# Optimization experiments

Hardware: AMD Instinct MI355X
Metric: run time of the kernel (lower is better)

Reference implementation:

```python
import jax, jax.numpy as jnp
import numpy as np

BETA = 0.25
EPS = 1e-12


def l2_normalize(x, axis=-1, eps=EPS):
    return x * jax.lax.rsqrt((x * x).sum(axis=axis, keepdims=True) + eps)


def setup_inputs() -> dict:
    key = jax.random.key(0)
    k1, k2 = jax.random.split(key)
    z = jax.random.normal(k1, (16, 32, 32, 256), dtype=jnp.float32)
    # embedding_init = uniform(2.0, -1.0) -> U[-1, 1)
    embedding = jax.random.uniform(k2, (8192, 256), dtype=jnp.float32) * 2.0 - 1.0
    return {"z": z, "embedding": embedding}


def reference(z, embedding):
    e_dim = embedding.shape[-1]
    z_flat = jnp.reshape(z, (-1, e_dim))                      # [N, D]
    z_flat_n = l2_normalize(z_flat, axis=-1)                  # [N, D]
    emb_n = l2_normalize(embedding, axis=-1)                  # [K, D]
    # squared L2 distance between normalized vectors
    d = (jnp.sum(z_flat_n ** 2, axis=1, keepdims=True)
         + jnp.sum(emb_n ** 2, axis=1)
         - 2.0 * jnp.einsum('nd,kd->nk', z_flat_n, emb_n))    # [N, K]
    min_idx = jnp.reshape(jnp.argmin(d, axis=1), z.shape[:-1])  # [B,H,W]
    # codebook lookup + renormalize
    z_q = l2_normalize(jnp.take(embedding, min_idx, axis=0), axis=-1)  # [B,H,W,D]
    z_norm = l2_normalize(z, axis=-1)
    loss = (BETA * jnp.mean(jnp.square(jax.lax.stop_gradient(z_q) - z_norm))
            + jnp.mean(jnp.square(z_q - jax.lax.stop_gradient(z_norm))))
    # straight-through estimator
    z_q_st = z + jax.lax.stop_gradient(z_q - z)
    return (z_q_st, loss, min_idx)
```

## Files before the change

kernel.cpp:

```cpp
#include <hip/hip_runtime.h>
#include <math.h>

#define D 256
#define NROW 16384
#define KCODE 8192
#define MARGIN 1.2e-3f

typedef _Float16 half8 __attribute__((ext_vector_type(8)));
typedef _Float16 half4f __attribute__((ext_vector_type(4)));
typedef __attribute__((ext_vector_type(4))) float f32x4;

__device__ __forceinline__ float dot4(float4 a, float4 b) {
  return a.x * b.x + a.y * b.y + a.z * b.z + a.w * b.w;
}
__device__ __forceinline__ float wave_sum(float s) {
#pragma unroll
  for (int off = 32; off; off >>= 1) s += __shfl_xor(s, off, 64);
  return s;
}
__device__ __forceinline__ float wave_min_f(float v) {
#pragma unroll
  for (int off = 32; off; off >>= 1) v = fminf(v, __shfl_xor(v, off, 64));
  return v;
}

__global__ __launch_bounds__(256) void k_prep(const float* __restrict__ emb,
                                              const float* __restrict__ z,
                                              float* __restrict__ emb_n,
                                              float* __restrict__ e2,
                                              _Float16* __restrict__ Bb,
                                              _Float16* __restrict__ Ab) {
  const int b = blockIdx.x;
  const int w = threadIdx.x >> 6, l = threadIdx.x & 63;
  const int ph = l >> 3;
  const int qd = (l & 7) >> 1;
  const int hf = l & 1;
  if (b < 2048) {
    int row = b * 4 + w;
    float4 v = ((const float4*)(emb + (size_t)row * D))[l];
    float s = wave_sum(dot4(v, v));
    float inv = 1.0f / sqrtf(s + 1e-12f);
    v.x *= inv; v.y *= inv; v.z *= inv; v.w *= inv;
    ((float4*)(emb_n + (size_t)row * D))[l] = v;
    float s2 = wave_sum(dot4(v, v));
    if (l == 0) e2[row] = s2;
    half4f h;
    h[0] = (_Float16)v.x; h[1] = (_Float16)v.y;
    h[2] = (_Float16)v.z; h[3] = (_Float16)v.w;
    int t = row >> 7, r = row & 127;
    size_t off = (size_t)t * 32768 + ph * 4096 + (r >> 6) * 2048 +
                 ((r >> 4) & 3) * 512 + (qd * 16 + (r & 15)) * 8 + hf * 4;
    *(half4f*)(Bb + off) = h;
  } else {
    int row = (b - 2048) * 4 + w;
    float4 v = ((const float4*)(z + (size_t)row * D))[l];
    float s = wave_sum(dot4(v, v));
    float inv = 1.0f / sqrtf(s + 1e-12f);
    v.x *= inv; v.y *= inv; v.z *= inv; v.w *= inv;
    half4f h;
    h[0] = (_Float16)v.x; h[1] = (_Float16)v.y;
    h[2] = (_Float16)v.z; h[3] = (_Float16)v.w;
    int t = row >> 7, r = row & 127;
    size_t off = (size_t)t * 32768 + ph * 4096 + (r >> 6) * 2048 +
                 ((r >> 4) & 3) * 512 + (qd * 16 + (r & 15)) * 8 + hf * 4;
    *(half4f*)(Ab + off) = h;
  }
}

__device__ __forceinline__ void merge2(float& d1, int& k1, float& d2, int& k2,
                                       float od1, int ok1, float od2, int ok2) {
  bool w1 = (od1 < d1) || (od1 == d1 && ok1 < k1);
  float n1 = w1 ? od1 : d1; int nk1 = w1 ? ok1 : k1;
  float c  = w1 ? d1 : od1; int ck  = w1 ? k1 : ok1;
  float c2 = w1 ? od2 : d2; int ck2 = w1 ? ok2 : k2;
  bool w2 = (c2 < c) || (c2 == c && ck2 < ck);
  d1 = n1; k1 = nk1;
  d2 = w2 ? c2 : c; k2 = w2 ? ck2 : ck;
}

__global__ __launch_bounds__(256, 3) void k_gemm_argmin10(
    const _Float16* __restrict__ Cb,
    const _Float16* __restrict__ Zb,
    const float* __restrict__ e2, float4* __restrict__ top2) {
  __shared__ float4 mbuf[256];
  const int tid = threadIdx.x, w = tid >> 6, l = tid & 63;
  const int wm = w >> 1, wn = w & 1;
  const int quad = l >> 4, col = l & 15;
  const int xcd = blockIdx.x & 7;
  const int j = blockIdx.x >> 3;
  const int ct = xcd * 8 + (j & 7);
  const int zt = j >> 3;
  const int c0 = ct * 128;

  const _Float16* At = Cb + (size_t)ct * 32768 + wm * 2048 + l * 8;
  const _Float16* Bt = Zb + (size_t)zt * 32768 + wn * 2048 + l * 8;

  f32x4 acc[4][4] = {};
  half8 a0[4], b0[4], a1[4], b1[4];
#pragma unroll
  for (int mf = 0; mf < 4; ++mf) {
    a0[mf] = *(const half8*)(At + mf * 512);
    b0[mf] = *(const half8*)(Bt + mf * 512);
  }
#pragma unroll
  for (int ph = 0; ph < 8; ph += 2) {
#pragma unroll
    for (int mf = 0; mf < 4; ++mf) {
      a1[mf] = *(const half8*)(At + (ph + 1) * 4096 + mf * 512);
      b1[mf] = *(const half8*)(Bt + (ph + 1) * 4096 + mf * 512);
    }
    __builtin_amdgcn_s_setprio(1);
#pragma unroll
    for (int mf = 0; mf < 4; ++mf)
#pragma unroll
      for (int nf = 0; nf < 4; ++nf)
        acc[mf][nf] = __builtin_amdgcn_mfma_f32_16x16x32_f16(a0[mf], b0[nf], acc[mf][nf], 0, 0, 0);
    __builtin_amdgcn_s_setprio(0);
    if (ph < 6) {
#pragma unroll
      for (int mf = 0; mf < 4; ++mf) {
        a0[mf] = *(const half8*)(At + (ph + 2) * 4096 + mf * 512);
        b0[mf] = *(const half8*)(Bt + (ph + 2) * 4096 + mf * 512);
      }
    }
    __builtin_amdgcn_s_setprio(1);
#pragma unroll
    for (int mf = 0; mf < 4; ++mf)
#pragma unroll
      for (int nf = 0; nf < 4; ++nf)
        acc[mf][nf] = __builtin_amdgcn_mfma_f32_16x16x32_f16(a1[mf], b1[nf], acc[mf][nf], 0, 0, 0);
    __builtin_amdgcn_s_setprio(0);
  }

  float e2r[16];
#pragma unroll
  for (int mf = 0; mf < 4; ++mf)
#pragma unroll
    for (int v = 0; v < 4; ++v)
      e2r[mf * 4 + v] = e2[c0 + wm * 64 + mf * 16 + quad * 4 + v];

#pragma unroll
  for (int nf = 0; nf < 4; ++nf) {
    float d1 = 1e30f, d2 = 1e30f; int k1 = 0, k2 = 0;
#pragma unroll
    for (int mf = 0; mf < 4; ++mf)
#pragma unroll
      for (int v = 0; v < 4; ++v) {
        float d = fmaf(-2.0f, acc[mf][nf][v], e2r[mf * 4 + v]);
        int kc = c0 + wm * 64 + mf * 16 + quad * 4 + v;
        bool lt1 = d < d1, lt2 = d < d2;
        d2 = lt1 ? d1 : (lt2 ? d : d2);
        k2 = lt1 ? k1 : (lt2 ? kc : k2);
        d1 = lt1 ? d : d1;
        k1 = lt1 ? kc : k1;
      }
#pragma unroll
    for (int m = 16; m < 64; m <<= 1) {
      float od1 = __shfl_xor(d1, m, 64); int ok1 = __shfl_xor(k1, m, 64);
      float od2 = __shfl_xor(d2, m, 64); int ok2 = __shfl_xor(k2, m, 64);
      merge2(d1, k1, d2, k2, od1, ok1, od2, ok2);
    }
    if (quad == 0)
      mbuf[(wm * 2 + wn) * 64 + nf * 16 + col] =
          make_float4(d1, d2, __int_as_float(k1), __int_as_float(k2));
  }
  __syncthreads();
  if (tid < 128) {
    const int wnn = tid >> 6, zc = tid & 63;
    float4 a = mbuf[(0 * 2 + wnn) * 64 + zc];
    float4 b = mbuf[(1 * 2 + wnn) * 64 + zc];
    float d1 = a.x, d2 = a.y; int k1 = __float_as_int(a.z), k2 = __float_as_int(a.w);
    merge2(d1, k1, d2, k2, b.x, __float_as_int(b.z), b.y, __float_as_int(b.w));
    top2[((size_t)zt * 64 + ct) * 128 + tid] =
        make_float4(d1, d2, __int_as_float(k1), __int_as_float(k2));
  }
}

__global__ __launch_bounds__(256) void k_refine_gather(
    const float* __restrict__ z, const float* __restrict__ emb_n,
    const float* __restrict__ e2, const float4* __restrict__ top2,
    float* __restrict__ out0, float* __restrict__ idx_out,
    float* __restrict__ lsum, int* __restrict__ wl_row,
    unsigned long long* __restrict__ wl_mask, double* __restrict__ wl_best,
    int* __restrict__ wl_bk, int* __restrict__ n_flag) {
  __shared__ float zr[4][D];
  __shared__ float4 t2s[4][64];
  const int t = threadIdx.x;
  const int w = t >> 6, l = t & 63;
  const int row = blockIdx.x * 4 + w;
  float4 zv = ((const float4*)(z + (size_t)row * D))[l];
  float s = wave_sum(dot4(zv, zv));
  float inv = 1.0f / sqrtf(s + 1e-12f);
  float4 zn = make_float4(zv.x * inv, zv.y * inv, zv.z * inv, zv.w * inv);
  ((float4*)zr[w])[l] = zn;
  {
    const int zt = (blockIdx.x * 4) >> 7;
    const int rb = (blockIdx.x * 4) & 127;
    t2s[t & 3][t >> 2] = top2[((size_t)zt * 64 + (t >> 2)) * 128 + rb + (t & 3)];
  }
  __syncthreads();

  float4 e = t2s[w][l];
  const float ad1 = e.x, ad2 = e.y;
  const int ck1 = __float_as_int(e.z), ck2 = __float_as_int(e.w);
  const float d1g = wave_min_f(ad1);
  const float win = d1g + 2.0f * MARGIN;

  double best = 1e300; int bk = 0x7fffffff;
  unsigned long long m1 = __ballot(ad1 <= win);
  unsigned long long m2 = __ballot(ad2 <= win);
#pragma unroll 1
  for (int slot = 0; slot < 2; ++slot) {
    unsigned long long mm = slot ? m2 : m1;
    while (mm) {
      int ln = __builtin_ctzll(mm); mm &= mm - 1;
      int k = __shfl(slot ? ck2 : ck1, ln, 64);
      float4 e4 = ((const float4*)(emb_n + (size_t)k * D))[l];
      float4 z4 = ((const float4*)zr[w])[l];
      double p = (double)e4.x * (double)z4.x + (double)e4.y * (double)z4.y +
                 (double)e4.z * (double)z4.z + (double)e4.w * (double)z4.w;
#pragma unroll
      for (int off = 32; off; off >>= 1) p += __shfl_xor(p, off, 64);
      double dd = (double)e2[k] - 2.0 * p;
      if (dd < best || (dd == best && k < bk)) { best = dd; bk = k; }
    }
  }
  float4 q = ((const float4*)(emb_n + (size_t)bk * D))[l];
  float4 o;
  o.x = zv.x + (q.x - zv.x); o.y = zv.y + (q.y - zv.y);
  o.z = zv.z + (q.z - zv.z); o.w = zv.w + (q.w - zv.w);
  ((float4*)(out0 + (size_t)row * D))[l] = o;
  float dx = q.x - zn.x, dy = q.y - zn.y, dz = q.z - zn.z, dw = q.w - zn.w;
  float lp = wave_sum(dx * dx + dy * dy + dz * dz + dw * dw);
  if (l == 0) {
    lsum[row] = lp;
    idx_out[row] = (float)bk;
    if (m2) {
      int p = atomicAdd(n_flag, 1);
      wl_row[p] = row; wl_mask[p] = m2; wl_best[p] = best; wl_bk[p] = bk;
    }
  }
}

__global__ __launch_bounds__(256) void k_rescan(
    const float* __restrict__ z, const float* __restrict__ emb_n,
    const float* __restrict__ e2, const int* __restrict__ wl_row,
    const unsigned long long* __restrict__ wl_mask,
    const double* __restrict__ wl_best, const int* __restrict__ wl_bk,
    const int* __restrict__ n_flag, float* __restrict__ idx_out,
    float* __restrict__ out0, float* __restrict__ lsum) {
  __shared__ float zr[D];
  __shared__ double ph[128];
  __shared__ double sd[4];
  __shared__ int si[4];
  __shared__ int s_bk;
  const int tid = threadIdx.x;
  const int nf = *n_flag;
  for (int wi = blockIdx.x; wi < nf; wi += gridDim.x) {
    const int row = wl_row[wi];
    unsigned long long mask = wl_mask[wi];
    __syncthreads();
    if (tid < 64) {
      float4 zv = ((const float4*)(z + (size_t)row * D))[tid];
      float s = wave_sum(dot4(zv, zv));
      float inv = 1.0f / sqrtf(s + 1e-12f);
      ((float4*)zr)[tid] = make_float4(zv.x * inv, zv.y * inv, zv.z * inv, zv.w * inv);
    }
    __syncthreads();
    double best = wl_best[wi]; int bk = wl_bk[wi];
    while (mask) {
      const int sl = __builtin_ctzll(mask); mask &= mask - 1;
      const int code = (sl << 7) + (tid & 127);
      const int half = tid >> 7;
      const float4* ev = (const float4*)(emb_n + (size_t)code * D) + half * 32;
      const float4* zf = ((const float4*)zr) + half * 32;
      double a0 = 0.0, a1 = 0.0;
#pragma unroll 8
      for (int i = 0; i < 32; i += 2) {
        float4 e0 = ev[i], e1 = ev[i + 1], z0 = zf[i], z1 = zf[i + 1];
        a0 += (double)e0.x * (double)z0.x + (double)e0.y * (double)z0.y +
              (double)e0.z * (double)z0.z + (double)e0.w * (double)z0.w;
        a1 += (double)e1.x * (double)z1.x + (double)e1.y * (double)z1.y +
              (double)e1.z * (double)z1.z + (double)e1.w * (double)z1.w;
      }
      double p = a0 + a1;
      if (half) ph[tid & 127] = p;
      __syncthreads();
      if (!half) {
        double dd = (double)e2[code] - 2.0 * (p + ph[tid]);
        if (dd < best || (dd == best && code < bk)) { best = dd; bk = code; }
      }
      __syncthreads();
    }
#pragma unroll
    for (int off = 32; off; off >>= 1) {
      double od = __shfl_xor(best, off, 64); int ok = __shfl_xor(bk, off, 64);
      if (od < best || (od == best && ok < bk)) { best = od; bk = ok; }
    }
    if ((tid & 63) == 0) { sd[tid >> 6] = best; si[tid >> 6] = bk; }
    __syncthreads();
    if (tid == 0) {
#pragma unroll
      for (int q = 1; q < 4; ++q)
        if (sd[q] < best || (sd[q] == best && si[q] < bk)) { best = sd[q]; bk = si[q]; }
      s_bk = bk;
      idx_out[row] = (float)bk;
    }
    __syncthreads();
    const int fk = s_bk;
    if (tid < 64) {
      float4 zv = ((const float4*)(z + (size_t)row * D))[tid];
      float4 zn = ((const float4*)zr)[tid];
      float4 q = ((const float4*)(emb_n + (size_t)fk * D))[tid];
      float4 o;
      o.x = zv.x + (q.x - zv.x); o.y = zv.y + (q.y - zv.y);
      o.z = zv.z + (q.z - zv.z); o.w = zv.w + (q.w - zv.w);
      ((float4*)(out0 + (size_t)row * D))[tid] = o;
      float dx = q.x - zn.x, dy = q.y - zn.y, dz = q.z - zn.z, dw = q.w - zn.w;
      float lp = wave_sum(dx * dx + dy * dy + dz * dz + dw * dw);
      if (tid == 0) lsum[row] = lp;
    }
  }
}

__global__ __launch_bounds__(256) void k_reduce(const float* __restrict__ lsum,
                                                float* __restrict__ loss_out,
                                                float inv_cnt) {
  __shared__ float ws4[4];
  float s = 0.0f;
  const float4* p = (const float4*)lsum;
  for (int i = threadIdx.x; i < NROW / 4; i += 256) {
    float4 v = p[i];
    s += (v.x + v.y) + (v.z + v.w);
  }
  s = wave_sum(s);
  if ((threadIdx.x & 63) == 0) ws4[threadIdx.x >> 6] = s;
  __syncthreads();
  if (threadIdx.x == 0) {
    float m = ((ws4[0] + ws4[1]) + (ws4[2] + ws4[3])) * inv_cnt;
    *loss_out = 0.25f * m + m;
  }
}

__device__ __forceinline__ int sw_f(int row, int d4) { return row * D + 4 * (d4 ^ (row & 7)); }
__global__ __launch_bounds__(256, 1) void k_argmin_f32(const float* __restrict__ z,
                                                       const float* __restrict__ emb_n,
                                                       const float* __restrict__ e2,
                                                       float* __restrict__ idx_out, int K) {
  extern __shared__ float smem[];
  float* zs = smem; float* es = smem + 64 * D;
  int tid = threadIdx.x; int w = tid >> 6, l = tid & 63;
  size_t r0 = (size_t)blockIdx.x * 64;
#pragma unroll
  for (int i = 0; i < 16; ++i) {
    int row = 4 * i + w;
    float4 v = ((const float4*)(z + (r0 + row) * D))[l];
    float s = wave_sum(dot4(v, v));
    float inv = 1.0f / sqrtf(s + 1e-12f);
    v.x *= inv; v.y *= inv; v.z *= inv; v.w *= inv;
    *(float4*)(&zs[sw_f(row, l)]) = v;
  }
  __syncthreads();
  int tc = tid & 15, tr = tid >> 4;
  float bestd[4] = {1e30f, 1e30f, 1e30f, 1e30f};
  int bestk[4] = {0, 0, 0, 0};
  for (int k0 = 0; k0 < K; k0 += 64) {
#pragma unroll
    for (int i = 0; i < 16; ++i) {
      int row = 4 * i + w;
      float4 v = ((const float4*)(emb_n + (size_t)(k0 + row) * D))[l];
      *(float4*)(&es[sw_f(row, l)]) = v;
    }
    __syncthreads();
    float acc[4][4] = {};
#pragma unroll 4
    for (int d4 = 0; d4 < 64; ++d4) {
      float4 zv[4], ev[4];
#pragma unroll
      for (int i = 0; i < 4; ++i) zv[i] = *(const float4*)(&zs[sw_f(tr + 16 * i, d4)]);
#pragma unroll
      for (int jx = 0; jx < 4; ++jx) ev[jx] = *(const float4*)(&es[sw_f(tc + 16 * jx, d4)]);
#pragma unroll
      for (int i = 0; i < 4; ++i)
#pragma unroll
        for (int jx = 0; jx < 4; ++jx)
          acc[i][jx] = fmaf(zv[i].x, ev[jx].x, fmaf(zv[i].y, ev[jx].y,
                       fmaf(zv[i].z, ev[jx].z, fmaf(zv[i].w, ev[jx].w, acc[i][jx]))));
    }
#pragma unroll
    for (int jx = 0; jx < 4; ++jx) {
      int k = k0 + tc + 16 * jx;
      float ek = e2[k];
#pragma unroll
      for (int i = 0; i < 4; ++i) {
        float dd = fmaf(-2.0f, acc[i][jx], ek);
        if (dd < bestd[i]) { bestd[i] = dd; bestk[i] = k; }
      }
    }
    __syncthreads();
  }
#pragma unroll
  for (int i = 0; i < 4; ++i) {
    float dd = bestd[i]; int kkk = bestk[i];
#pragma unroll
    for (int off = 1; off < 16; off <<= 1) {
      float od = __shfl_xor(dd, off, 64); int ok = __shfl_xor(kkk, off, 64);
      if (od < dd || (od == dd && ok < kkk)) { dd = od; kkk = ok; }
    }
    if (tc == 0) idx_out[r0 + tr + 16 * i] = (float)kkk;
  }
}

__global__ __launch_bounds__(256) void k_gather(const float* __restrict__ z,
                                                const float* __restrict__ emb_n,
                                                const float* __restrict__ idx_f,
                                                float* __restrict__ out0,
                                                float* __restrict__ loss_acc) {
  __shared__ float wsum[4];
  int w = threadIdx.x >> 6, l = threadIdx.x & 63;
  int row = blockIdx.x * 4 + w;
  float4 zv = ((const float4*)(z + (size_t)row * D))[l];
  float s = wave_sum(dot4(zv, zv));
  float inv = 1.0f / sqrtf(s + 1e-12f);
  int k = (int)idx_f[row];
  float4 q = ((const float4*)(emb_n + (size_t)k * D))[l];
  float4 o;
  o.x = zv.x + (q.x - zv.x); o.y = zv.y + (q.y - zv.y);
  o.z = zv.z + (q.z - zv.z); o.w = zv.w + (q.w - zv.w);
  ((float4*)(out0 + (size_t)row * D))[l] = o;
  float dx = q.x - zv.x * inv, dy = q.y - zv.y * inv;
  float dz = q.z - zv.z * inv, dw = q.w - zv.w * inv;
  float lp = wave_sum(dx * dx + dy * dy + dz * dz + dw * dw);
  if (l == 0) wsum[w] = lp;
  __syncthreads();
  if (threadIdx.x == 0) atomicAdd(loss_acc, wsum[0] + wsum[1] + wsum[2] + wsum[3]);
}

__global__ void k_final(const float* __restrict__ loss_acc,
                        float* __restrict__ loss_out, float inv_cnt) {
  float m = *loss_acc * inv_cnt;
  *loss_out = 0.25f * m + m;
}

extern "C" void kernel_launch(void* const* d_in, const int* in_sizes, int n_in,
                              void* d_out, int out_size, void* d_ws, size_t ws_size,
                              hipStream_t stream) {
  const float* z = (const float*)d_in[0];
  const float* emb = (const float*)d_in[1];
  int N = in_sizes[0] / D;
  int K = in_sizes[1] / D;

  float* out0 = (float*)d_out;
  float* loss_out = out0 + (size_t)N * D;
  float* idx_out = loss_out + 1;

  char* ws = (char*)d_ws;
  float* emb_n = (float*)ws;
  float* e2 = (float*)(ws + 8388608);
  float* loss_acc = (float*)(ws + 8421376);
  int* n_flag = (int*)(ws + 8421380);
  float* lsum = (float*)(ws + 8421392);
  _Float16* Bb = (_Float16*)(ws + 8486928);
  _Float16* Ab = (_Float16*)(ws + 12681232);
  float4* top2 = (float4*)(ws + 21069840);
  const size_t NEED = 37847056;
  int* wl_row = (int*)Ab;
  unsigned long long* wl_mask = (unsigned long long*)((char*)Ab + 65536);
  double* wl_best = (double*)((char*)Ab + 196608);
  int* wl_bk = (int*)((char*)Ab + 327680);

  const float inv_cnt = 1.0f / (float)((size_t)N * D);
  hipMemsetAsync(loss_acc, 0, 8, stream);
  if (ws_size >= NEED) {
    k_prep<<<K / 4 + N / 4, 256, 0, stream>>>(emb, z, emb_n, e2, Bb, Ab);
    k_gemm_argmin10<<<(K / 128) * (N / 128), 256, 0, stream>>>(Bb, Ab, e2, top2);
    k_refine_gather<<<N / 4, 256, 0, stream>>>(z, emb_n, e2, top2, out0, idx_out,
                                               lsum, wl_row, wl_mask, wl_best,
                                               wl_bk, n_flag);
    k_rescan<<<1024, 256, 0, stream>>>(z, emb_n, e2, wl_row, wl_mask, wl_best,
                                       wl_bk, n_flag, idx_out, out0, lsum);
    k_reduce<<<1, 256, 0, stream>>>(lsum, loss_out, inv_cnt);
  } else {
    k_prep<<<K / 4 + N / 4, 256, 0, stream>>>(emb, z, emb_n, e2, Bb, Ab);
    k_argmin_f32<<<N / 64, 256, 131072, stream>>>(z, emb_n, e2, idx_out, K);
    k_gather<<<N / 4, 256, 0, stream>>>(z, emb_n, idx_out, out0, loss_acc);
    k_final<<<1, 1, 0, stream>>>(loss_acc, loss_out, inv_cnt);
  }
}
```

Before: 198.8 us.

## Switch distance GEMM to 32x32x16 MFMA with matching fp16 operand layout

Replaces the 16x16x32 MFMA tiles in the fused GEMM+top-2 kernel with 32x32x16 MFMAs, and changes the fp16 packed layout written by the prep kernel to match the new operand fragments. Fewer, larger MFMAs cut instruction count and operand register loads per FLOP, and the top-2 reduction needs only one cross-lane shuffle stage. Occupancy hint rises from 3 to 4 blocks per CU, which may increase register pressure or spilling given the 16-wide accumulators.

```diff
diff --git a/kernel.cpp b/kernel.cpp
--- a/kernel.cpp
+++ b/kernel.cpp
@@ -9,6 +9,7 @@
 typedef _Float16 half8 __attribute__((ext_vector_type(8)));
 typedef _Float16 half4f __attribute__((ext_vector_type(4)));
 typedef __attribute__((ext_vector_type(4))) float f32x4;
+typedef __attribute__((ext_vector_type(16))) float f32x16;
 
 __device__ __forceinline__ float dot4(float4 a, float4 b) {
   return a.x * b.x + a.y * b.y + a.z * b.z + a.w * b.w;
@@ -32,8 +33,8 @@
                                               _Float16* __restrict__ Ab) {
   const int b = blockIdx.x;
   const int w = threadIdx.x >> 6, l = threadIdx.x & 63;
-  const int ph = l >> 3;
-  const int qd = (l & 7) >> 1;
+  const int kf = l >> 2;
+  const int kg = (l >> 1) & 1;
   const int hf = l & 1;
   if (b < 2048) {
     int row = b * 4 + w;
@@ -48,8 +49,8 @@
     h[0] = (_Float16)v.x; h[1] = (_Float16)v.y;
     h[2] = (_Float16)v.z; h[3] = (_Float16)v.w;
     int t = row >> 7, r = row & 127;
-    size_t off = (size_t)t * 32768 + ph * 4096 + (r >> 6) * 2048 +
-                 ((r >> 4) & 3) * 512 + (qd * 16 + (r & 15)) * 8 + hf * 4;
+    size_t off = (size_t)t * 32768 + kf * 2048 + (r >> 5) * 512 +
+                 (kg * 32 + (r & 31)) * 8 + hf * 4;
     *(half4f*)(Bb + off) = h;
   } else {
     int row = (b - 2048) * 4 + w;
@@ -61,8 +62,8 @@
     h[0] = (_Float16)v.x; h[1] = (_Float16)v.y;
     h[2] = (_Float16)v.z; h[3] = (_Float16)v.w;
     int t = row >> 7, r = row & 127;
-    size_t off = (size_t)t * 32768 + ph * 4096 + (r >> 6) * 2048 +
-                 ((r >> 4) & 3) * 512 + (qd * 16 + (r & 15)) * 8 + hf * 4;
+    size_t off = (size_t)t * 32768 + kf * 2048 + (r >> 5) * 512 +
+                 (kg * 32 + (r & 31)) * 8 + hf * 4;
     *(half4f*)(Ab + off) = h;
   }
 }
@@ -78,99 +79,110 @@
   d2 = w2 ? c2 : c; k2 = w2 ? ck2 : ck;
 }
 
-__global__ __launch_bounds__(256, 3) void k_gemm_argmin10(
+__global__ __launch_bounds__(256, 4) void k_gemm_argmin11(
     const _Float16* __restrict__ Cb,
     const _Float16* __restrict__ Zb,
     const float* __restrict__ e2, float4* __restrict__ top2) {
   __shared__ float4 mbuf[256];
   const int tid = threadIdx.x, w = tid >> 6, l = tid & 63;
   const int wm = w >> 1, wn = w & 1;
-  const int quad = l >> 4, col = l & 15;
+  const int hi = l >> 5, ln31 = l & 31;
   const int xcd = blockIdx.x & 7;
   const int j = blockIdx.x >> 3;
   const int ct = xcd * 8 + (j & 7);
   const int zt = j >> 3;
   const int c0 = ct * 128;
 
-  const _Float16* At = Cb + (size_t)ct * 32768 + wm * 2048 + l * 8;
-  const _Float16* Bt = Zb + (size_t)zt * 32768 + wn * 2048 + l * 8;
-
-  f32x4 acc[4][4] = {};
-  half8 a0[4], b0[4], a1[4], b1[4];
-#pragma unroll
-  for (int mf = 0; mf < 4; ++mf) {
-    a0[mf] = *(const half8*)(At + mf * 512);
-    b0[mf] = *(const half8*)(Bt + mf * 512);
-  }
-#pragma unroll
-  for (int ph = 0; ph < 8; ph += 2) {
-#pragma unroll
-    for (int mf = 0; mf < 4; ++mf) {
-      a1[mf] = *(const half8*)(At + (ph + 1) * 4096 + mf * 512);
-      b1[mf] = *(const half8*)(Bt + (ph + 1) * 4096 + mf * 512);
+  const _Float16* At = Cb + (size_t)ct * 32768 + (wm * 2) * 512 + (size_t)l * 8;
+  const _Float16* Bt = Zb + (size_t)zt * 32768 + (wn * 2) * 512 + (size_t)l * 8;
+
+  f32x16 acc[2][2] = {};
+  half8 aA[4], aB[4], b[4];
+
+#pragma unroll
+  for (int x = 0; x < 2; ++x)
+#pragma unroll
+    for (int sub = 0; sub < 2; ++sub) {
+      aA[x * 2 + sub] = *(const half8*)(At + x * 512 + sub * 2048);
+      b[x * 2 + sub]  = *(const half8*)(Bt + x * 512 + sub * 2048);
+    }
+
+#pragma unroll
+  for (int ph = 0; ph < 8; ++ph) {
+    half8* ac = (ph & 1) ? aB : aA;
+    half8* an = (ph & 1) ? aA : aB;
+    if (ph < 7) {
+#pragma unroll
+      for (int mf = 0; mf < 2; ++mf)
+#pragma unroll
+        for (int sub = 0; sub < 2; ++sub)
+          an[mf * 2 + sub] = *(const half8*)(At + mf * 512 + (2 * (ph + 1) + sub) * 2048);
     }
     __builtin_amdgcn_s_setprio(1);
-#pragma unroll
-    for (int mf = 0; mf < 4; ++mf)
-#pragma unroll
-      for (int nf = 0; nf < 4; ++nf)
-        acc[mf][nf] = __builtin_amdgcn_mfma_f32_16x16x32_f16(a0[mf], b0[nf], acc[mf][nf], 0, 0, 0);
+    acc[0][0] = __builtin_amdgcn_mfma_f32_32x32x16_f16(ac[0], b[0], acc[0][0], 0, 0, 0);
+    acc[0][1] = __builtin_amdgcn_mfma_f32_32x32x16_f16(ac[0], b[2], acc[0][1], 0, 0, 0);
+    acc[1][0] = __builtin_amdgcn_mfma_f32_32x32x16_f16(ac[2], b[0], acc[1][0], 0, 0, 0);
+    acc[1][1] = __builtin_amdgcn_mfma_f32_32x32x16_f16(ac[2], b[2], acc[1][1], 0, 0, 0);
     __builtin_amdgcn_s_setprio(0);
-    if (ph < 6) {
-#pragma unroll
-      for (int mf = 0; mf < 4; ++mf) {
-        a0[mf] = *(const half8*)(At + (ph + 2) * 4096 + mf * 512);
-        b0[mf] = *(const half8*)(Bt + (ph + 2) * 4096 + mf * 512);
+    if (ph < 7) {
+      b[0] = *(const half8*)(Bt + 0 * 512 + (2 * (ph + 1) + 0) * 2048);
+      b[2] = *(const half8*)(Bt + 1 * 512 + (2 * (ph + 1) + 0) * 2048);
+    }
+    __builtin_amdgcn_s_setprio(1);
+    acc[0][0] = __builtin_amdgcn_mfma_f32_32x32x16_f16(ac[1], b[1], acc[0][0], 0, 0, 0);
+    acc[0][1] = __builtin_amdgcn_mfma_f32_32x32x16_f16(ac[1], b[3], acc[0][1], 0, 0, 0);
+    acc[1][0] = __builtin_amdgcn_mfma_f32_32x32x16_f16(ac[3], b[1], acc[1][0], 0, 0, 0);
+    acc[1][1] = __builtin_amdgcn_mfma_f32_32x32x16_f16(ac[3], b[3], acc[1][1], 0, 0, 0);
+    __builtin_amdgcn_s_setprio(0);
+    if (ph < 7) {
+      b[1] = *(const half8*)(Bt + 0 * 512 + (2 * (ph + 1) + 1) * 2048);
+      b[3] = *(const half8*)(Bt + 1 * 512 + (2 * (ph + 1) + 1) * 2048);
+    }
+  }
+
+  float4 e2v[2][4];
+#pragma unroll
+  for (int mf = 0; mf < 2; ++mf)
+#pragma unroll
+    for (int rg = 0; rg < 4; ++rg)
+      e2v[mf][rg] = *(const float4*)(e2 + c0 + wm * 64 + mf * 32 + rg * 8 + 4 * hi);
+
+#pragma unroll
+  for (int nf = 0; nf < 2; ++nf) {
+    float d1 = 1e30f, d2 = 1e30f; int k1 = 0, k2 = 0;
+#pragma unroll
+    for (int mf = 0; mf < 2; ++mf)
+#pragma unroll
+      for (int rg = 0; rg < 4; ++rg) {
+        float4 ev = e2v[mf][rg];
+#pragma unroll
+        for (int v = 0; v < 4; ++v) {
+          float evv = (v == 0) ? ev.x : (v == 1) ? ev.y : (v == 2) ? ev.z : ev.w;
+          float d = fmaf(-2.0f, acc[mf][nf][rg * 4 + v], evv);
+          int kc = c0 + wm * 64 + mf * 32 + rg * 8 + 4 * hi + v;
+          bool lt1 = d < d1, lt2 = d < d2;
+          d2 = lt1 ? d1 : (lt2 ? d : d2);
+          k2 = lt1 ? k1 : (lt2 ? kc : k2);
+          d1 = lt1 ? d : d1;
+          k1 = lt1 ? kc : k1;
+        }
       }
-    }
-    __builtin_amdgcn_s_setprio(1);
-#pragma unroll
-    for (int mf = 0; mf < 4; ++mf)
-#pragma unroll
-      for (int nf = 0; nf < 4; ++nf)
-        acc[mf][nf] = __builtin_amdgcn_mfma_f32_16x16x32_f16(a1[mf], b1[nf], acc[mf][nf], 0, 0, 0);
-    __builtin_amdgcn_s_setprio(0);
-  }
-
-  float e2r[16];
-#pragma unroll
-  for (int mf = 0; mf < 4; ++mf)
-#pragma unroll
-    for (int v = 0; v < 4; ++v)
-      e2r[mf * 4 + v] = e2[c0 + wm * 64 + mf * 16 + quad * 4 + v];
-
-#pragma unroll
-  for (int nf = 0; nf < 4; ++nf) {
-    float d1 = 1e30f, d2 = 1e30f; int k1 = 0, k2 = 0;
-#pragma unroll
-    for (int mf = 0; mf < 4; ++mf)
-#pragma unroll
-      for (int v = 0; v < 4; ++v) {
-        float d = fmaf(-2.0f, acc[mf][nf][v], e2r[mf * 4 + v]);
-        int kc = c0 + wm * 64 + mf * 16 + quad * 4 + v;
-        bool lt1 = d < d1, lt2 = d < d2;
-        d2 = lt1 ? d1 : (lt2 ? d : d2);
-        k2 = lt1 ? k1 : (lt2 ? kc : k2);
-        d1 = lt1 ? d : d1;
-        k1 = lt1 ? kc : k1;
-      }
-#pragma unroll
-    for (int m = 16; m < 64; m <<= 1) {
-      float od1 = __shfl_xor(d1, m, 64); int ok1 = __shfl_xor(k1, m, 64);
-      float od2 = __shfl_xor(d2, m, 64); int ok2 = __shfl_xor(k2, m, 64);
+    {
+      float od1 = __shfl_xor(d1, 32, 64); int ok1 = __shfl_xor(k1, 32, 64);
+      float od2 = __shfl_xor(d2, 32, 64); int ok2 = __shfl_xor(k2, 32, 64);
       merge2(d1, k1, d2, k2, od1, ok1, od2, ok2);
     }
-    if (quad == 0)
-      mbuf[(wm * 2 + wn) * 64 + nf * 16 + col] =
+    if (hi == 0)
+      mbuf[(wm * 2 + wn) * 64 + nf * 32 + ln31] =
           make_float4(d1, d2, __int_as_float(k1), __int_as_float(k2));
   }
   __syncthreads();
   if (tid < 128) {
     const int wnn = tid >> 6, zc = tid & 63;
     float4 a = mbuf[(0 * 2 + wnn) * 64 + zc];
-    float4 b = mbuf[(1 * 2 + wnn) * 64 + zc];
+    float4 bb = mbuf[(1 * 2 + wnn) * 64 + zc];
     float d1 = a.x, d2 = a.y; int k1 = __float_as_int(a.z), k2 = __float_as_int(a.w);
-    merge2(d1, k1, d2, k2, b.x, __float_as_int(b.z), b.y, __float_as_int(b.w));
+    merge2(d1, k1, d2, k2, bb.x, __float_as_int(bb.z), bb.y, __float_as_int(bb.w));
     top2[((size_t)zt * 64 + ct) * 128 + tid] =
         make_float4(d1, d2, __int_as_float(k1), __int_as_float(k2));
   }
@@ -473,7 +485,7 @@
   hipMemsetAsync(loss_acc, 0, 8, stream);
   if (ws_size >= NEED) {
     k_prep<<<K / 4 + N / 4, 256, 0, stream>>>(emb, z, emb_n, e2, Bb, Ab);
-    k_gemm_argmin10<<<(K / 128) * (N / 128), 256, 0, stream>>>(Bb, Ab, e2, top2);
+    k_gemm_argmin11<<<(K / 128) * (N / 128), 256, 0, stream>>>(Bb, Ab, e2, top2);
     k_refine_gather<<<N / 4, 256, 0, stream>>>(z, emb_n, e2, top2, out0, idx_out,
                                                lsum, wl_row, wl_mask, wl_best,
                                                wl_bk, n_flag);
```

Result: slower. 260.7 us (+31.2%).

## Stage codebook tile in LDS via async global-to-LDS loads in GEMM-argmin

Applied to the files above, without the earlier changes.

The GEMM+argmin kernel now copies the whole 128x256 fp16 codebook tile into shared memory with global_load_lds async copies up front. Each wave then reads its A fragments from LDS, so the A tile is fetched from global memory once per block instead of once per wave pair. Z fragments still come straight from global memory, double-buffered in registers. This needs 64 KB of LDS, so the occupancy hint drops from 3 to 2 blocks per CU. The result buffer now reuses that LDS region after a sync.

```diff
diff --git a/kernel.cpp b/kernel.cpp
--- a/kernel.cpp
+++ b/kernel.cpp
@@ -22,6 +22,11 @@
 #pragma unroll
   for (int off = 32; off; off >>= 1) v = fminf(v, __shfl_xor(v, off, 64));
   return v;
+}
+__device__ __forceinline__ void async16(const void* g, void* l) {
+  __builtin_amdgcn_global_load_lds(
+      (const __attribute__((address_space(1))) unsigned int*)g,
+      (__attribute__((address_space(3))) unsigned int*)l, 16, 0, 0);
 }
 
 __global__ __launch_bounds__(256) void k_prep(const float* __restrict__ emb,
@@ -78,11 +83,11 @@
   d2 = w2 ? c2 : c; k2 = w2 ? ck2 : ck;
 }
 
-__global__ __launch_bounds__(256, 3) void k_gemm_argmin10(
+__global__ __launch_bounds__(256, 2) void k_gemm_argmin16(
     const _Float16* __restrict__ Cb,
     const _Float16* __restrict__ Zb,
     const float* __restrict__ e2, float4* __restrict__ top2) {
-  __shared__ float4 mbuf[256];
+  __shared__ _Float16 As[32768];
   const int tid = threadIdx.x, w = tid >> 6, l = tid & 63;
   const int wm = w >> 1, wn = w & 1;
   const int quad = l >> 4, col = l & 15;
@@ -92,45 +97,71 @@
   const int zt = j >> 3;
   const int c0 = ct * 128;
 
-  const _Float16* At = Cb + (size_t)ct * 32768 + wm * 2048 + l * 8;
-  const _Float16* Bt = Zb + (size_t)zt * 32768 + wn * 2048 + l * 8;
+  const _Float16* Bt = Zb + (size_t)zt * 32768 + wn * 2048 + (size_t)l * 8;
 
   f32x4 acc[4][4] = {};
-  half8 a0[4], b0[4], a1[4], b1[4];
-#pragma unroll
-  for (int mf = 0; mf < 4; ++mf) {
-    a0[mf] = *(const half8*)(At + mf * 512);
-    b0[mf] = *(const half8*)(Bt + mf * 512);
-  }
-#pragma unroll
-  for (int ph = 0; ph < 8; ph += 2) {
-#pragma unroll
-    for (int mf = 0; mf < 4; ++mf) {
-      a1[mf] = *(const half8*)(At + (ph + 1) * 4096 + mf * 512);
-      b1[mf] = *(const half8*)(Bt + (ph + 1) * 4096 + mf * 512);
-    }
-    __builtin_amdgcn_s_setprio(1);
-#pragma unroll
-    for (int mf = 0; mf < 4; ++mf)
-#pragma unroll
-      for (int nf = 0; nf < 4; ++nf)
-        acc[mf][nf] = __builtin_amdgcn_mfma_f32_16x16x32_f16(a0[mf], b0[nf], acc[mf][nf], 0, 0, 0);
-    __builtin_amdgcn_s_setprio(0);
-    if (ph < 6) {
-#pragma unroll
-      for (int mf = 0; mf < 4; ++mf) {
-        a0[mf] = *(const half8*)(At + (ph + 2) * 4096 + mf * 512);
-        b0[mf] = *(const half8*)(Bt + (ph + 2) * 4096 + mf * 512);
-      }
-    }
-    __builtin_amdgcn_s_setprio(1);
-#pragma unroll
-    for (int mf = 0; mf < 4; ++mf)
-#pragma unroll
-      for (int nf = 0; nf < 4; ++nf)
-        acc[mf][nf] = __builtin_amdgcn_mfma_f32_16x16x32_f16(a1[mf], b1[nf], acc[mf][nf], 0, 0, 0);
-    __builtin_amdgcn_s_setprio(0);
-  }
+  half8 bU0, bU1, bU2, bU3, bV0, bV1, bV2, bV3;
+
+  {
+    const _Float16* gA = Cb + (size_t)ct * 32768;
+#pragma unroll
+    for (int k = 0; k < 16; ++k)
+      async16(gA + (size_t)(k * 256 + tid) * 8, (char*)As + (size_t)(k * 256 + tid) * 16);
+  }
+  __builtin_amdgcn_sched_barrier(0);
+  bU0 = *(const half8*)(Bt + 0 * 512);
+  bU1 = *(const half8*)(Bt + 1 * 512);
+  bU2 = *(const half8*)(Bt + 2 * 512);
+  bU3 = *(const half8*)(Bt + 3 * 512);
+  __builtin_amdgcn_sched_barrier(0);
+  asm volatile("s_waitcnt vmcnt(4)" ::: "memory");
+  __builtin_amdgcn_s_barrier();
+  __builtin_amdgcn_sched_barrier(0);
+
+#define KPH16(CB0, CB1, CB2, CB3, NB0, NB1, NB2, NB3, PH)                     \
+  {                                                                           \
+    if ((PH) < 7) {                                                           \
+      NB0 = *(const half8*)(Bt + ((PH) + 1) * 4096 + 0 * 512);                \
+      NB1 = *(const half8*)(Bt + ((PH) + 1) * 4096 + 1 * 512);                \
+      NB2 = *(const half8*)(Bt + ((PH) + 1) * 4096 + 2 * 512);                \
+      NB3 = *(const half8*)(Bt + ((PH) + 1) * 4096 + 3 * 512);                \
+    }                                                                         \
+    half8 af0 = *(const half8*)(As + (PH) * 4096 + wm * 2048 + 0 * 512 + l * 8); \
+    half8 af1 = *(const half8*)(As + (PH) * 4096 + wm * 2048 + 1 * 512 + l * 8); \
+    half8 af2 = *(const half8*)(As + (PH) * 4096 + wm * 2048 + 2 * 512 + l * 8); \
+    half8 af3 = *(const half8*)(As + (PH) * 4096 + wm * 2048 + 3 * 512 + l * 8); \
+    __builtin_amdgcn_s_setprio(1);                                            \
+    acc[0][0] = __builtin_amdgcn_mfma_f32_16x16x32_f16(af0, CB0, acc[0][0], 0, 0, 0); \
+    acc[0][1] = __builtin_amdgcn_mfma_f32_16x16x32_f16(af0, CB1, acc[0][1], 0, 0, 0); \
+    acc[0][2] = __builtin_amdgcn_mfma_f32_16x16x32_f16(af0, CB2, acc[0][2], 0, 0, 0); \
+    acc[0][3] = __builtin_amdgcn_mfma_f32_16x16x32_f16(af0, CB3, acc[0][3], 0, 0, 0); \
+    acc[1][0] = __builtin_amdgcn_mfma_f32_16x16x32_f16(af1, CB0, acc[1][0], 0, 0, 0); \
+    acc[1][1] = __builtin_amdgcn_mfma_f32_16x16x32_f16(af1, CB1, acc[1][1], 0, 0, 0); \
+    acc[1][2] = __builtin_amdgcn_mfma_f32_16x16x32_f16(af1, CB2, acc[1][2], 0, 0, 0); \
+    acc[1][3] = __builtin_amdgcn_mfma_f32_16x16x32_f16(af1, CB3, acc[1][3], 0, 0, 0); \
+    acc[2][0] = __builtin_amdgcn_mfma_f32_16x16x32_f16(af2, CB0, acc[2][0], 0, 0, 0); \
+    acc[2][1] = __builtin_amdgcn_mfma_f32_16x16x32_f16(af2, CB1, acc[2][1], 0, 0, 0); \
+    acc[2][2] = __builtin_amdgcn_mfma_f32_16x16x32_f16(af2, CB2, acc[2][2], 0, 0, 0); \
+    acc[2][3] = __builtin_amdgcn_mfma_f32_16x16x32_f16(af2, CB3, acc[2][3], 0, 0, 0); \
+    acc[3][0] = __builtin_amdgcn_mfma_f32_16x16x32_f16(af3, CB0, acc[3][0], 0, 0, 0); \
+    acc[3][1] = __builtin_amdgcn_mfma_f32_16x16x32_f16(af3, CB1, acc[3][1], 0, 0, 0); \
+    acc[3][2] = __builtin_amdgcn_mfma_f32_16x16x32_f16(af3, CB2, acc[3][2], 0, 0, 0); \
+    acc[3][3] = __builtin_amdgcn_mfma_f32_16x16x32_f16(af3, CB3, acc[3][3], 0, 0, 0); \
+    __builtin_amdgcn_s_setprio(0);                                            \
+  }
+
+  KPH16(bU0, bU1, bU2, bU3, bV0, bV1, bV2, bV3, 0)
+  KPH16(bV0, bV1, bV2, bV3, bU0, bU1, bU2, bU3, 1)
+  KPH16(bU0, bU1, bU2, bU3, bV0, bV1, bV2, bV3, 2)
+  KPH16(bV0, bV1, bV2, bV3, bU0, bU1, bU2, bU3, 3)
+  KPH16(bU0, bU1, bU2, bU3, bV0, bV1, bV2, bV3, 4)
+  KPH16(bV0, bV1, bV2, bV3, bU0, bU1, bU2, bU3, 5)
+  KPH16(bU0, bU1, bU2, bU3, bV0, bV1, bV2, bV3, 6)
+  KPH16(bV0, bV1, bV2, bV3, bU0, bU1, bU2, bU3, 7)
+#undef KPH16
+
+  __syncthreads();
+  float4* mbuf = (float4*)As;
 
   float e2r[16];
 #pragma unroll
@@ -473,7 +504,7 @@
   hipMemsetAsync(loss_acc, 0, 8, stream);
   if (ws_size >= NEED) {
     k_prep<<<K / 4 + N / 4, 256, 0, stream>>>(emb, z, emb_n, e2, Bb, Ab);
-    k_gemm_argmin10<<<(K / 128) * (N / 128), 256, 0, stream>>>(Bb, Ab, e2, top2);
+    k_gemm_argmin16<<<(K / 128) * (N / 128), 256, 0, stream>>>(Bb, Ab, e2, top2);
     k_refine_gather<<<N / 4, 256, 0, stream>>>(z, emb_n, e2, top2, out0, idx_out,
                                                lsum, wl_row, wl_mask, wl_best,
                                                wl_bk, n_flag);
```

New measurement: 210.3 us. 1.06x slower.
